# Kernel tuning notes

Hardware: AMD Instinct MI355X
Metric: run time of the kernel (lower is better)

Reference implementation:

```python
import jax, jax.numpy as jnp
import numpy as np


def setup_inputs() -> dict:
    key = jax.random.key(0)
    k1, k2 = jax.random.split(key)
    decoder_hidden = jax.random.normal(k1, (16, 1024, 1024), dtype=jnp.float32)
    encoder_outputs = jax.random.normal(k2, (16, 2048, 1024), dtype=jnp.float32)
    return {"decoder_hidden": decoder_hidden, "encoder_outputs": encoder_outputs}


def reference(decoder_hidden, encoder_outputs):
    # scores: [B, Q, K] = decoder_hidden @ encoder_outputs^T (no scaling, per source)
    scores = jnp.einsum('bqd,bkd->bqk', decoder_hidden, encoder_outputs)
    attn = jax.nn.softmax(scores, axis=-1)
    # context: [B, Q, D]
    context = jnp.einsum('bqk,bkd->bqd', attn, encoder_outputs)
    return (context, attn)
```

## Files before the change

kernel.cpp:

```cpp
#include <hip/hip_runtime.h>


typedef __attribute__((ext_vector_type(8))) short s8v;
typedef __attribute__((ext_vector_type(4))) float f32x4;
typedef __attribute__((ext_vector_type(8))) unsigned short us8;
typedef __attribute__((ext_vector_type(4))) unsigned short us4;

__device__ inline unsigned short f2bf(float f) {
    unsigned u = __builtin_bit_cast(unsigned, f);
    u += 0x7FFFu + ((u >> 16) & 1u);
    return (unsigned short)(u >> 16);
}
__device__ inline float bf2f(unsigned short h) {
    return __builtin_bit_cast(float, (unsigned)h << 16);
}

__device__ __forceinline__ s8v lds_read128(unsigned addr) {
    s8v d;
    asm volatile("ds_read_b128 %0, %1" : "=v"(d) : "v"(addr));
    return d;
}

__global__ __launch_bounds__(256)
void split_convert(const float* __restrict__ x, unsigned short* __restrict__ hi,
                   unsigned short* __restrict__ lo, int n4)
{
    int i = blockIdx.x * 256 + threadIdx.x;
    const int stride = gridDim.x * 256;
    for (; i < n4; i += stride) {
        const float4 v = reinterpret_cast<const float4*>(x)[i];
        us4 h, l;
        h.x = f2bf(v.x); l.x = f2bf(v.x - bf2f(h.x));
        h.y = f2bf(v.y); l.y = f2bf(v.y - bf2f(h.y));
        h.z = f2bf(v.z); l.z = f2bf(v.z - bf2f(h.z));
        h.w = f2bf(v.w); l.w = f2bf(v.w - bf2f(h.w));
        reinterpret_cast<us4*>(hi)[i] = h;
        reinterpret_cast<us4*>(lo)[i] = l;
    }
}

__global__ __launch_bounds__(256)
void transpose_bf16(const unsigned short* __restrict__ in, unsigned short* __restrict__ out)
{
    __shared__ unsigned short S[64][72];
    const int b  = blockIdx.z;
    const int kt = blockIdx.x;
    const int dt = blockIdx.y;
    const unsigned short* ib = in  + (size_t)b * 2048 * 1024 + (size_t)kt * 64 * 1024 + (size_t)dt * 64;
    unsigned short*       ob = out + (size_t)b * 1024 * 2048 + (size_t)dt * 64 * 2048 + (size_t)kt * 64;

    const int tid = threadIdx.x;
    const int r0 = tid >> 3, c8 = (tid & 7) * 8;
    #pragma unroll
    for (int p = 0; p < 2; ++p) {
        const int r = r0 + 32 * p;
        const us8 v = *reinterpret_cast<const us8*>(&ib[(size_t)r * 1024 + c8]);
        *reinterpret_cast<us8*>(&S[r][c8]) = v;
    }
    __syncthreads();
    const int d0 = tid >> 3, k8 = (tid & 7) * 8;
    #pragma unroll
    for (int p = 0; p < 2; ++p) {
        const int d = d0 + 32 * p;
        us8 w;
        #pragma unroll
        for (int j = 0; j < 8; ++j) w[j] = S[k8 + j][d];
        *reinterpret_cast<us8*>(&ob[(size_t)d * 2048 + k8]) = w;
    }
}

template<int NPASS, int KPP, int NXT, int NYT>
__global__ __launch_bounds__(512, 2)
void gemm_nt_256(const unsigned short* __restrict__ A0,
                 const unsigned short* __restrict__ A1,
                 const unsigned short* __restrict__ A2,
                 const unsigned short* __restrict__ B0,
                 const unsigned short* __restrict__ B1,
                 const unsigned short* __restrict__ B2,
                 float* __restrict__ Out,
                 const int ldA, const int ldB, const int ldO,
                 const long long sA, const long long sB, const long long sO)
{
    constexpr int TPP = KPP / 32;
    constexpr int NT  = NPASS * TPP;
    extern __shared__ unsigned short smem[];

    int flat = blockIdx.x + NXT * (blockIdx.y + NYT * (int)blockIdx.z);
    const int nwg = NXT * NYT * (int)gridDim.z;
    flat = (flat & 7) * (nwg >> 3) + (flat >> 3);
    const int nt = flat % NXT;
    const int mt = (flat / NXT) % NYT;
    const int b  = flat / (NXT * NYT);

    const int tid = threadIdx.x, lane = tid & 63, wid = tid >> 6;
    const int wm = wid >> 2, wn = wid & 3;

    const size_t arow = (size_t)b * sA + (size_t)(mt * 256) * ldA;
    const size_t brow = (size_t)b * sB + (size_t)(nt * 256) * ldB;
    const unsigned short* Ap0 = A0 + arow;
    const unsigned short* Ap1 = A1 + arow;
    const unsigned short* Ap2 = A2 + arow;
    const unsigned short* Bp0 = B0 + brow;
    const unsigned short* Bp1 = B1 + brow;
    const unsigned short* Bp2 = B2 + brow;

    const int ci0 = tid, ci1 = 512 + tid;
    const int r0 = ci0 >> 2, r1 = ci1 >> 2;
    const int cs0 = ((ci0 & 3) ^ ((r0 >> 1) & 3)) * 8;
    const int cs1 = ((ci1 & 3) ^ ((r1 >> 1) & 3)) * 8;
    const int aoff0 = r0 * ldA + cs0, aoff1 = r1 * ldA + cs1;
    const int boff0 = r0 * ldB + cs0, boff1 = r1 * ldB + cs1;
    const int wd0 = wid * 512;
    const int wd1 = 4096 + wid * 512;

    auto stageA = [&](int t) {
        const int p  = t / TPP;
        const int k0 = (t % TPP) * 32;
        const unsigned short* As = (p == 0) ? Ap0 : (p == 1 ? Ap1 : Ap2);
        unsigned short* d = smem + (t & 3) * 16384;
        __builtin_amdgcn_global_load_lds(
            (const __attribute__((address_space(1))) void*)(As + k0 + aoff0),
            (__attribute__((address_space(3))) void*)(d + wd0), 16, 0, 0);
        __builtin_amdgcn_global_load_lds(
            (const __attribute__((address_space(1))) void*)(As + k0 + aoff1),
            (__attribute__((address_space(3))) void*)(d + wd1), 16, 0, 0);
    };
    auto stageB = [&](int t) {
        const int p  = t / TPP;
        const int k0 = (t % TPP) * 32;
        const unsigned short* Bs = (p == 0) ? Bp0 : (p == 1 ? Bp1 : Bp2);
        unsigned short* d = smem + (t & 3) * 16384 + 8192;
        __builtin_amdgcn_global_load_lds(
            (const __attribute__((address_space(1))) void*)(Bs + k0 + boff0),
            (__attribute__((address_space(3))) void*)(d + wd0), 16, 0, 0);
        __builtin_amdgcn_global_load_lds(
            (const __attribute__((address_space(1))) void*)(Bs + k0 + boff1),
            (__attribute__((address_space(3))) void*)(d + wd1), 16, 0, 0);
    };

    const int fr = lane & 15;
    const int kc = lane >> 4;
    unsigned offA[8], offB[4];
    #pragma unroll
    for (int m = 0; m < 8; ++m) {
        const int R = wm * 128 + m * 16 + fr;
        offA[m] = (unsigned)(R * 64) + ((unsigned)(kc ^ ((R >> 1) & 3)) << 4);
    }
    #pragma unroll
    for (int n = 0; n < 4; ++n) {
        const int R = wn * 64 + n * 16 + fr;
        offB[n] = 16384u + (unsigned)(R * 64) + ((unsigned)(kc ^ ((R >> 1) & 3)) << 4);
    }

    const unsigned lds0 =
        (unsigned)(uintptr_t)(__attribute__((address_space(3))) unsigned short*)smem;

    f32x4 acc[8][4];
    #pragma unroll
    for (int m = 0; m < 8; ++m)
        #pragma unroll
        for (int n = 0; n < 4; ++n) acc[m][n] = (f32x4){0.f, 0.f, 0.f, 0.f};

    stageA(0); stageB(0); stageA(1); stageB(1); stageA(2); stageB(2);
    asm volatile("s_waitcnt vmcnt(8)" ::: "memory");
    __builtin_amdgcn_s_barrier();

    for (int t = 0; t < NT; ++t) {
        const unsigned base = lds0 + (unsigned)(t & 3) * 32768u;
        s8v a[8], bb[4];

        #pragma unroll
        for (int n = 0; n < 4; ++n) bb[n] = lds_read128(base + offB[n]);
        #pragma unroll
        for (int m = 0; m < 4; ++m) a[m] = lds_read128(base + offA[m]);
        if (t + 3 < NT) stageA(t + 3);
        __builtin_amdgcn_s_barrier();
        asm volatile("s_waitcnt lgkmcnt(0)" ::: "memory");
        __builtin_amdgcn_sched_barrier(0);
        __builtin_amdgcn_s_setprio(1);
        #pragma unroll
        for (int m = 0; m < 4; ++m)
            #pragma unroll
            for (int n = 0; n < 4; ++n)
                acc[m][n] = __builtin_amdgcn_mfma_f32_16x16x32_bf16(a[m], bb[n], acc[m][n], 0, 0, 0);
        __builtin_amdgcn_s_setprio(0);
        __builtin_amdgcn_s_barrier();

        #pragma unroll
        for (int m = 4; m < 8; ++m) a[m] = lds_read128(base + offA[m]);
        if (t + 3 < NT) stageB(t + 3);
        __builtin_amdgcn_s_barrier();
        asm volatile("s_waitcnt lgkmcnt(0)" ::: "memory");
        __builtin_amdgcn_sched_barrier(0);
        __builtin_amdgcn_s_setprio(1);
        #pragma unroll
        for (int m = 4; m < 8; ++m)
            #pragma unroll
            for (int n = 0; n < 4; ++n)
                acc[m][n] = __builtin_amdgcn_mfma_f32_16x16x32_bf16(a[m], bb[n], acc[m][n], 0, 0, 0);
        __builtin_amdgcn_s_setprio(0);

        const int rem = NT - 1 - t;
        if (rem >= 3)      asm volatile("s_waitcnt vmcnt(8)" ::: "memory");
        else if (rem == 2) asm volatile("s_waitcnt vmcnt(4)" ::: "memory");
        else if (rem == 1) asm volatile("s_waitcnt vmcnt(0)" ::: "memory");
        __builtin_amdgcn_s_barrier();
    }

    float* Ob = Out + (size_t)b * sO + (size_t)(mt * 256 + wm * 128) * ldO + nt * 256 + wn * 64;
    const int cr = (lane >> 4) << 2;
    const int cc = lane & 15;
    #pragma unroll
    for (int m = 0; m < 8; ++m)
        #pragma unroll
        for (int n = 0; n < 4; ++n)
            #pragma unroll
            for (int r = 0; r < 4; ++r)
                Ob[(size_t)(m * 16 + cr + r) * ldO + n * 16 + cc] = acc[m][n][r];
}

__global__ __launch_bounds__(256)
void softmax_rows_bf(float* __restrict__ P, unsigned short* __restrict__ Pb)
{
    float* p = P + (size_t)blockIdx.x * 2048;
    unsigned short* pb = Pb + (size_t)blockIdx.x * 2048;
    const int tid = threadIdx.x;

    float4 v0 = *reinterpret_cast<const float4*>(&p[tid * 4]);
    float4 v1 = *reinterpret_cast<const float4*>(&p[1024 + tid * 4]);

    float m = fmaxf(fmaxf(fmaxf(v0.x, v0.y), fmaxf(v0.z, v0.w)),
                    fmaxf(fmaxf(v1.x, v1.y), fmaxf(v1.z, v1.w)));
    #pragma unroll
    for (int off = 32; off; off >>= 1) m = fmaxf(m, __shfl_xor(m, off));

    __shared__ float red[8];
    const int wid = tid >> 6;
    if ((tid & 63) == 0) red[wid] = m;
    __syncthreads();
    m = fmaxf(fmaxf(red[0], red[1]), fmaxf(red[2], red[3]));

    v0.x = __expf(v0.x - m); v0.y = __expf(v0.y - m);
    v0.z = __expf(v0.z - m); v0.w = __expf(v0.w - m);
    v1.x = __expf(v1.x - m); v1.y = __expf(v1.y - m);
    v1.z = __expf(v1.z - m); v1.w = __expf(v1.w - m);

    float s = ((v0.x + v0.y) + (v0.z + v0.w)) + ((v1.x + v1.y) + (v1.z + v1.w));
    #pragma unroll
    for (int off = 32; off; off >>= 1) s += __shfl_xor(s, off);
    if ((tid & 63) == 0) red[4 + wid] = s;
    __syncthreads();
    const float inv = 1.0f / ((red[4] + red[5]) + (red[6] + red[7]));

    v0.x *= inv; v0.y *= inv; v0.z *= inv; v0.w *= inv;
    v1.x *= inv; v1.y *= inv; v1.z *= inv; v1.w *= inv;
    *reinterpret_cast<float4*>(&p[tid * 4]) = v0;
    *reinterpret_cast<float4*>(&p[1024 + tid * 4]) = v1;

    us4 h0, h1;
    h0.x = f2bf(v0.x); h0.y = f2bf(v0.y); h0.z = f2bf(v0.z); h0.w = f2bf(v0.w);
    h1.x = f2bf(v1.x); h1.y = f2bf(v1.y); h1.z = f2bf(v1.z); h1.w = f2bf(v1.w);
    *reinterpret_cast<us4*>(&pb[tid * 4]) = h0;
    *reinterpret_cast<us4*>(&pb[1024 + tid * 4]) = h1;
}

#define BM 128
#define BN 128
#define BK 32
#define LDT 132

template <bool TRANSB>
__global__ __launch_bounds__(256, 2)
void gemm_tile(const float* __restrict__ X, const float* __restrict__ Y,
               float* __restrict__ Out,
               int ldX, int ldY, int ldO, int KD,
               long long strideX, long long strideY, long long strideO)
{
    __shared__ float As[BK][LDT];
    __shared__ float Bs[BK][LDT];
    const int b  = blockIdx.z;
    const int mt = blockIdx.y;
    const int nt = blockIdx.x;
    const float* Xb = X + (size_t)b * strideX + (size_t)mt * BM * ldX;
    const float* Yb = TRANSB ? (Y + (size_t)b * strideY + (size_t)nt * BN * ldY)
                             : (Y + (size_t)b * strideY + (size_t)nt * BN);
    float* Ob = Out + (size_t)b * strideO + (size_t)mt * BM * ldO + (size_t)nt * BN;
    const int tid = threadIdx.x;
    const int tx = tid & 15;
    const int ty = tid >> 4;
    const int sr = tid >> 3;
    const int sc = (tid & 7) << 2;
    const int br = tid >> 5;
    const int bc = (tid & 31) << 2;
    float acc[8][8];
    #pragma unroll
    for (int i = 0; i < 8; ++i)
        #pragma unroll
        for (int j = 0; j < 8; ++j) acc[i][j] = 0.f;
    for (int k0 = 0; k0 < KD; k0 += BK) {
        #pragma unroll
        for (int p = 0; p < 4; ++p) {
            const float4 v = *reinterpret_cast<const float4*>(
                &Xb[(size_t)(sr + 32 * p) * ldX + k0 + sc]);
            As[sc + 0][sr + 32 * p] = v.x;
            As[sc + 1][sr + 32 * p] = v.y;
            As[sc + 2][sr + 32 * p] = v.z;
            As[sc + 3][sr + 32 * p] = v.w;
        }
        if (TRANSB) {
            #pragma unroll
            for (int p = 0; p < 4; ++p) {
                const float4 v = *reinterpret_cast<const float4*>(
                    &Yb[(size_t)(sr + 32 * p) * ldY + k0 + sc]);
                Bs[sc + 0][sr + 32 * p] = v.x;
                Bs[sc + 1][sr + 32 * p] = v.y;
                Bs[sc + 2][sr + 32 * p] = v.z;
                Bs[sc + 3][sr + 32 * p] = v.w;
            }
        } else {
            #pragma unroll
            for (int p = 0; p < 4; ++p) {
                const float4 v = *reinterpret_cast<const float4*>(
                    &Yb[(size_t)(k0 + br + 8 * p) * ldY + bc]);
                *reinterpret_cast<float4*>(&Bs[br + 8 * p][bc]) = v;
            }
        }
        __syncthreads();
        #pragma unroll 8
        for (int kk = 0; kk < BK; ++kk) {
            const float4 a0 = *reinterpret_cast<const float4*>(&As[kk][ty * 4]);
            const float4 a1 = *reinterpret_cast<const float4*>(&As[kk][64 + ty * 4]);
            const float4 b0 = *reinterpret_cast<const float4*>(&Bs[kk][tx * 4]);
            const float4 b1 = *reinterpret_cast<const float4*>(&Bs[kk][64 + tx * 4]);
            const float av[8] = {a0.x, a0.y, a0.z, a0.w, a1.x, a1.y, a1.z, a1.w};
            const float bv[8] = {b0.x, b0.y, b0.z, b0.w, b1.x, b1.y, b1.z, b1.w};
            #pragma unroll
            for (int i = 0; i < 8; ++i)
                #pragma unroll
                for (int j = 0; j < 8; ++j)
                    acc[i][j] = fmaf(av[i], bv[j], acc[i][j]);
        }
        __syncthreads();
    }
    #pragma unroll
    for (int i = 0; i < 8; ++i) {
        const int r = (i < 4) ? (ty * 4 + i) : (64 + ty * 4 + (i - 4));
        const float4 w0 = make_float4(acc[i][0], acc[i][1], acc[i][2], acc[i][3]);
        const float4 w1 = make_float4(acc[i][4], acc[i][5], acc[i][6], acc[i][7]);
        *reinterpret_cast<float4*>(&Ob[(size_t)r * ldO + tx * 4])      = w0;
        *reinterpret_cast<float4*>(&Ob[(size_t)r * ldO + 64 + tx * 4]) = w1;
    }
}

__global__ __launch_bounds__(256)
void softmax_rows(float* __restrict__ P)
{
    float* p = P + (size_t)blockIdx.x * 2048;
    const int tid = threadIdx.x;
    float4 v0 = *reinterpret_cast<const float4*>(&p[tid * 4]);
    float4 v1 = *reinterpret_cast<const float4*>(&p[1024 + tid * 4]);
    float m = fmaxf(fmaxf(fmaxf(v0.x, v0.y), fmaxf(v0.z, v0.w)),
                    fmaxf(fmaxf(v1.x, v1.y), fmaxf(v1.z, v1.w)));
    #pragma unroll
    for (int off = 32; off; off >>= 1) m = fmaxf(m, __shfl_xor(m, off));
    __shared__ float red[8];
    const int wid = tid >> 6;
    if ((tid & 63) == 0) red[wid] = m;
    __syncthreads();
    m = fmaxf(fmaxf(red[0], red[1]), fmaxf(red[2], red[3]));
    v0.x = __expf(v0.x - m); v0.y = __expf(v0.y - m);
    v0.z = __expf(v0.z - m); v0.w = __expf(v0.w - m);
    v1.x = __expf(v1.x - m); v1.y = __expf(v1.y - m);
    v1.z = __expf(v1.z - m); v1.w = __expf(v1.w - m);
    float s = ((v0.x + v0.y) + (v0.z + v0.w)) + ((v1.x + v1.y) + (v1.z + v1.w));
    #pragma unroll
    for (int off = 32; off; off >>= 1) s += __shfl_xor(s, off);
    if ((tid & 63) == 0) red[4 + wid] = s;
    __syncthreads();
    const float inv = 1.0f / ((red[4] + red[5]) + (red[6] + red[7]));
    v0.x *= inv; v0.y *= inv; v0.z *= inv; v0.w *= inv;
    v1.x *= inv; v1.y *= inv; v1.z *= inv; v1.w *= inv;
    *reinterpret_cast<float4*>(&p[tid * 4]) = v0;
    *reinterpret_cast<float4*>(&p[1024 + tid * 4]) = v1;
}

extern "C" void kernel_launch(void* const* d_in, const int* in_sizes, int n_in,
                              void* d_out, int out_size, void* d_ws, size_t ws_size,
                              hipStream_t stream)
{
    const float* dec = (const float*)d_in[0];
    const float* enc = (const float*)d_in[1];
    float* ctx  = (float*)d_out;
    float* attn = ctx + (size_t)16 * 1024 * 1024;

    const long long DECN = 16LL * 1024 * 1024;
    const long long ENCN = 16LL * 2048 * 1024;
    const size_t NEED = (size_t)(2 * DECN + 4 * ENCN) * 2;

    if (ws_size >= NEED) {
        unsigned short* decH  = (unsigned short*)d_ws;
        unsigned short* decL  = decH + DECN;
        unsigned short* encH  = decL + DECN;
        unsigned short* encL  = encH + ENCN;
        unsigned short* encT  = encL + ENCN;
        unsigned short* attnB = encT + ENCN;

        hipFuncSetAttribute((const void*)&gemm_nt_256<3, 1024, 8, 4>,
                            hipFuncAttributeMaxDynamicSharedMemorySize, 131072);
        hipFuncSetAttribute((const void*)&gemm_nt_256<1, 2048, 4, 4>,
                            hipFuncAttributeMaxDynamicSharedMemorySize, 131072);

        split_convert<<<2048, 256, 0, stream>>>(dec, decH, decL, (int)(DECN / 4));
        split_convert<<<2048, 256, 0, stream>>>(enc, encH, encL, (int)(ENCN / 4));
        transpose_bf16<<<dim3(32, 16, 16), 256, 0, stream>>>(encH, encT);

        gemm_nt_256<3, 1024, 8, 4><<<dim3(8, 4, 16), 512, 131072, stream>>>(
            decH, decH, decL, encH, encL, encH, attn,
            1024, 1024, 2048,
            1024LL * 1024, 2048LL * 1024, 1024LL * 2048);

        softmax_rows_bf<<<16 * 1024, 256, 0, stream>>>(attn, attnB);

        gemm_nt_256<1, 2048, 4, 4><<<dim3(4, 4, 16), 512, 131072, stream>>>(
            attnB, attnB, attnB, encT, encT, encT, ctx,
            2048, 2048, 1024,
            1024LL * 2048, 1024LL * 2048, 1024LL * 1024);
    } else {
        gemm_tile<true><<<dim3(2048 / BN, 1024 / BM, 16), 256, 0, stream>>>(
            dec, enc, attn, 1024, 1024, 2048, 1024,
            1024LL * 1024, 2048LL * 1024, 1024LL * 2048);
        softmax_rows<<<dim3(16 * 1024), 256, 0, stream>>>(attn);
        gemm_tile<false><<<dim3(1024 / BN, 1024 / BM, 16), 256, 0, stream>>>(
            attn, enc, ctx, 2048, 1024, 1024, 2048,
            1024LL * 2048, 2048LL * 1024, 1024LL * 1024);
    }
}
```

Measured before the change: 433.1 us.

## Double-buffer register fragments to overlap LDS reads with MFMA in GEMM loop

Restructures the GEMM main loop so that LDS fragments for tile t+1 are read into a second register set while the MFMAs for tile t run, with the loop unrolled by two to ping-pong between register sets. It merges the two half-tile phases into one, dropping two of the three barriers per iteration, and issues both global stages together. The cost is higher register pressure from holding two fragment sets, a deeper vmcnt wait that assumes NT is even, and different barrier placement that could change LDS reuse safety.

```diff
diff --git a/kernel.cpp b/kernel.cpp
--- a/kernel.cpp
+++ b/kernel.cpp
@@ -162,49 +162,44 @@
         for (int n = 0; n < 4; ++n) acc[m][n] = (f32x4){0.f, 0.f, 0.f, 0.f};
 
     stageA(0); stageB(0); stageA(1); stageB(1); stageA(2); stageB(2);
-    asm volatile("s_waitcnt vmcnt(8)" ::: "memory");
+    asm volatile("s_waitcnt vmcnt(4)" ::: "memory");
     __builtin_amdgcn_s_barrier();
 
-    for (int t = 0; t < NT; ++t) {
-        const unsigned base = lds0 + (unsigned)(t & 3) * 32768u;
-        s8v a[8], bb[4];
-
-        #pragma unroll
-        for (int n = 0; n < 4; ++n) bb[n] = lds_read128(base + offB[n]);
-        #pragma unroll
-        for (int m = 0; m < 4; ++m) a[m] = lds_read128(base + offA[m]);
-        if (t + 3 < NT) stageA(t + 3);
-        __builtin_amdgcn_s_barrier();
-        asm volatile("s_waitcnt lgkmcnt(0)" ::: "memory");
+    s8v fA[8], fB[4], gA[8], gB[4];
+    #pragma unroll
+    for (int n = 0; n < 4; ++n) fB[n] = lds_read128(lds0 + offB[n]);
+    #pragma unroll
+    for (int m = 0; m < 8; ++m) fA[m] = lds_read128(lds0 + offA[m]);
+
+    auto tile_body = [&](const int t, s8v (&ca)[8], s8v (&cb)[4],
+                         s8v (&na)[8], s8v (&nb)[4]) {
+        if (t + 3 < NT) { stageA(t + 3); stageB(t + 3); }
+        if (t + 1 < NT) {
+            const unsigned nbase = lds0 + (unsigned)((t + 1) & 3) * 32768u;
+            #pragma unroll
+            for (int n = 0; n < 4; ++n) nb[n] = lds_read128(nbase + offB[n]);
+            #pragma unroll
+            for (int m = 0; m < 8; ++m) na[m] = lds_read128(nbase + offA[m]);
+            asm volatile("s_waitcnt lgkmcnt(12)" ::: "memory");
+        } else {
+            asm volatile("s_waitcnt lgkmcnt(0)" ::: "memory");
+        }
         __builtin_amdgcn_sched_barrier(0);
         __builtin_amdgcn_s_setprio(1);
         #pragma unroll
-        for (int m = 0; m < 4; ++m)
+        for (int m = 0; m < 8; ++m)
             #pragma unroll
             for (int n = 0; n < 4; ++n)
-                acc[m][n] = __builtin_amdgcn_mfma_f32_16x16x32_bf16(a[m], bb[n], acc[m][n], 0, 0, 0);
+                acc[m][n] = __builtin_amdgcn_mfma_f32_16x16x32_bf16(ca[m], cb[n], acc[m][n], 0, 0, 0);
         __builtin_amdgcn_s_setprio(0);
+        if (t + 3 < NT)      asm volatile("s_waitcnt vmcnt(4)" ::: "memory");
+        else if (t + 2 < NT) asm volatile("s_waitcnt vmcnt(0)" ::: "memory");
         __builtin_amdgcn_s_barrier();
-
-        #pragma unroll
-        for (int m = 4; m < 8; ++m) a[m] = lds_read128(base + offA[m]);
-        if (t + 3 < NT) stageB(t + 3);
-        __builtin_amdgcn_s_barrier();
-        asm volatile("s_waitcnt lgkmcnt(0)" ::: "memory");
-        __builtin_amdgcn_sched_barrier(0);
-        __builtin_amdgcn_s_setprio(1);
-        #pragma unroll
-        for (int m = 4; m < 8; ++m)
-            #pragma unroll
-            for (int n = 0; n < 4; ++n)
-                acc[m][n] = __builtin_amdgcn_mfma_f32_16x16x32_bf16(a[m], bb[n], acc[m][n], 0, 0, 0);
-        __builtin_amdgcn_s_setprio(0);
-
-        const int rem = NT - 1 - t;
-        if (rem >= 3)      asm volatile("s_waitcnt vmcnt(8)" ::: "memory");
-        else if (rem == 2) asm volatile("s_waitcnt vmcnt(4)" ::: "memory");
-        else if (rem == 1) asm volatile("s_waitcnt vmcnt(0)" ::: "memory");
-        __builtin_amdgcn_s_barrier();
+    };
+
+    for (int tt = 0; tt < NT; tt += 2) {
+        tile_body(tt,     fA, fB, gA, gB);
+        tile_body(tt + 1, gA, gB, fA, fB);
     }
 
     float* Ob = Out + (size_t)b * sO + (size_t)(mt * 256 + wm * 128) * ldO + nt * 256 + wn * 64;
```

Result: no change. 427.5 us (-1.3%).
